# Kernel optimization log

Hardware: AMD Instinct MI355X
Metric: run time of the kernel (lower is better)

## Reference

```python
import jax, jax.numpy as jnp
import numpy as np
from jax.scipy.linalg import expm

NUM_QUBITS = 10
D = 2 ** NUM_QUBITS  # 1024
B, S = 8, 4096


def setup_inputs() -> dict:
    key = jax.random.key(0)
    k_x, k_mr, k_mi = jax.random.split(key, 3)
    inputs = jax.random.normal(k_x, (B, S, D), dtype=jnp.float32)
    M_real = 0.1 * jax.random.normal(k_mr, (D, D), dtype=jnp.float32)
    M_imag = 0.1 * jax.random.normal(k_mi, (D, D), dtype=jnp.float32)
    bias = jnp.zeros((D,), dtype=jnp.float32)
    qubit_gate = jnp.ones((D,), dtype=jnp.float32)
    return {"inputs": inputs, "M_real": M_real, "M_imag": M_imag,
            "bias": bias, "qubit_gate": qubit_gate}


def _l2_normalize(x, axis=-1, eps=1e-12):
    # matches tf.linalg.l2_normalize: x * rsqrt(max(sum(x^2), eps))
    ss = jnp.sum(jnp.square(x), axis=axis, keepdims=True)
    return x * jax.lax.rsqrt(jnp.maximum(ss, eps))


def reference(inputs, M_real, M_imag, bias, qubit_gate):
    norm_inputs = _l2_normalize(inputs, axis=-1)
    A = M_real - M_real.T  # skew-symmetric -> expm(A) is orthogonal
    Bm = M_imag - M_imag.T
    U = expm(A) @ expm(Bm)  # [D, D]
    transformed = jnp.einsum('bsd,de->bse', norm_inputs, U) + bias
    measured = jnp.square(transformed)
    gate_probs = jax.nn.softmax(qubit_gate)  # [D]
    gated_output = measured * gate_probs
    return gated_output, gate_probs
```

## Files before the change

kernel.cpp:

```cpp
#include <hip/hip_runtime.h>


typedef unsigned int u32;
typedef unsigned short u16;
typedef __attribute__((ext_vector_type(8))) short short8;
typedef __attribute__((ext_vector_type(4))) float f32x4;

#define GLOBAL_AS __attribute__((address_space(1)))
#define LDS_AS    __attribute__((address_space(3)))

constexpr int D = 1024;
constexpr float EXPM_SCALE = 1.0f / 4.0f;

__device__ __forceinline__ u16 f2bf(float f) {
  union { float f; u32 u; } v; v.f = f;
  u32 r = (v.u + 0x7FFFu + ((v.u >> 16) & 1u)) >> 16;
  return (u16)r;
}
__device__ __forceinline__ float bf2f(u16 u) {
  union { u32 u; float f; } v; v.u = ((u32)u) << 16;
  return v.f;
}

__device__ __forceinline__ void g2l16(const void* g, void* l) {
  __builtin_amdgcn_global_load_lds((const GLOBAL_AS u32*)g, (LDS_AS u32*)l,
                                   16, 0, 0);
}

#define WAITV(N)                                                   \
  do {                                                             \
    asm volatile("s_waitcnt vmcnt(" #N ")" ::: "memory");          \
    __builtin_amdgcn_sched_barrier(0);                             \
  } while (0)

__device__ void norm_rows8(const float* __restrict__ x, u16* __restrict__ Xn,
                           int r0, int tid, float* sred) {
  float4 v[8];
#pragma unroll
  for (int i = 0; i < 8; ++i)
    v[i] = ((const float4*)(x + (size_t)(r0 + i) * D))[tid];
  float ss[8];
#pragma unroll
  for (int i = 0; i < 8; ++i)
    ss[i] = v[i].x * v[i].x + v[i].y * v[i].y + v[i].z * v[i].z +
            v[i].w * v[i].w;
  for (int o = 32; o; o >>= 1)
#pragma unroll
    for (int i = 0; i < 8; ++i) ss[i] += __shfl_down(ss[i], o);
  const int w = tid >> 6;
  if ((tid & 63) == 0)
#pragma unroll
    for (int i = 0; i < 8; ++i) sred[i * 4 + w] = ss[i];
  __syncthreads();
#pragma unroll
  for (int i = 0; i < 8; ++i) {
    const float tot =
        sred[i * 4 + 0] + sred[i * 4 + 1] + sred[i * 4 + 2] + sred[i * 4 + 3];
    const float inv = rsqrtf(fmaxf(tot, 1e-12f));
    ushort4 o4;
    o4.x = f2bf(v[i].x * inv); o4.y = f2bf(v[i].y * inv);
    o4.z = f2bf(v[i].z * inv); o4.w = f2bf(v[i].w * inv);
    ((ushort4*)(Xn + (size_t)(r0 + i) * D))[tid] = o4;
  }
}

struct SkewParams {
  const float *Mr, *Mi;
  u16 *X0, *X1;
  const float* x;
  u16* Xn;
  int row0;
};
__global__ __launch_bounds__(256) void skew_norm_kernel(SkewParams p) {
  __shared__ __align__(16) float t2[64][67];
  const int bid = blockIdx.x, tid = threadIdx.x;
  if (bid >= 512) {
    norm_rows8(p.x, p.Xn, p.row0 + (bid - 512) * 8, tid, &t2[0][0]);
    return;
  }
  const int z = bid >> 8, t = bid & 255;
  const float* M = z ? p.Mi : p.Mr;
  u16* X = z ? p.X1 : p.X0;
  const int bi = t >> 4, bj = t & 15;
  const int r0 = tid >> 4, c0 = (tid & 15) * 4;
  float4 own[4];
#pragma unroll
  for (int i = 0; i < 4; ++i) {
    const int r = i * 16 + r0;
    own[i] = *(const float4*)(M + (size_t)(bi * 64 + r) * D + bj * 64 + c0);
    const float4 tr =
        *(const float4*)(M + (size_t)(bj * 64 + r) * D + bi * 64 + c0);
    t2[r][c0 + 0] = tr.x; t2[r][c0 + 1] = tr.y;
    t2[r][c0 + 2] = tr.z; t2[r][c0 + 3] = tr.w;
  }
  __syncthreads();
#pragma unroll
  for (int i = 0; i < 4; ++i) {
    const int r = i * 16 + r0;
    const float o[4] = {own[i].x, own[i].y, own[i].z, own[i].w};
    ushort4 hv;
    u16* hp = (u16*)&hv;
#pragma unroll
    for (int j = 0; j < 4; ++j)
      hp[j] = f2bf((o[j] - t2[c0 + j][r]) * EXPM_SCALE);
    *(ushort4*)(X + (size_t)(bi * 64 + r) * D + bj * 64 + c0) = hv;
  }
}

struct CJob {
  const u16 *A, *B;
  const float* C;
  u16 *Dst, *DT;
  float alpha;
};
struct GNParams {
  CJob jobs[2];
  int njobs;
  const float* x;
  u16* Xn;
  int row0;
};
__global__ __launch_bounds__(256) void gemm_norm_kernel(GNParams p) {
  __shared__ __align__(16) u16 ldsA[3][4096];
  __shared__ __align__(16) u16 ldsB[3][4096];
  const int bid = blockIdx.x, tid = threadIdx.x;
  if (bid >= p.njobs) {
    norm_rows8(p.x, p.Xn, p.row0 + (bid - p.njobs) * 8, tid,
               (float*)&ldsA[0][0]);
    return;
  }
  const CJob jb = p.jobs[bid >> 8];
  const int bi = (bid >> 4) & 15, bj = bid & 15;
  const int w = tid >> 6, lane = tid & 63;
  const int wr = w >> 1, wc = w & 1;
  f32x4 acc[2][2];
#pragma unroll
  for (int m = 0; m < 2; ++m)
#pragma unroll
    for (int n = 0; n < 2; ++n) acc[m][n] = f32x4{0.f, 0.f, 0.f, 0.f};
  const int r_l = lane >> 3, c_l = lane & 7;

  auto stage = [&](int buf, int kt) {
    const int k0 = kt * 64;
#pragma unroll
    for (int pp = 0; pp < 2; ++pp) {
      const int row = pp * 32 + w * 8 + r_l;
      const int chunk = c_l ^ (row & 7);
      g2l16(jb.A + (size_t)(bi * 64 + row) * D + k0 + chunk * 8,
            (char*)&ldsA[buf][0] + pp * 4096 + w * 1024);
      g2l16(jb.B + (size_t)(bj * 64 + row) * D + k0 + chunk * 8,
            (char*)&ldsB[buf][0] + pp * 4096 + w * 1024);
    }
  };
  auto compute = [&](int buf) {
#pragma unroll
    for (int h = 0; h < 2; ++h) {
      const int kk = h * 32 + (lane >> 4) * 8;
      short8 a[2], b[2];
#pragma unroll
      for (int m = 0; m < 2; ++m) {
        const int row = wr * 32 + m * 16 + (lane & 15);
        const int off = row * 128 + ((kk * 2) ^ ((row & 7) << 4));
        a[m] = *(const short8*)((const char*)&ldsA[buf][0] + off);
      }
#pragma unroll
      for (int n = 0; n < 2; ++n) {
        const int row = wc * 32 + n * 16 + (lane & 15);
        const int off = row * 128 + ((kk * 2) ^ ((row & 7) << 4));
        b[n] = *(const short8*)((const char*)&ldsB[buf][0] + off);
      }
#pragma unroll
      for (int m = 0; m < 2; ++m)
#pragma unroll
        for (int n = 0; n < 2; ++n)
          acc[m][n] = __builtin_amdgcn_mfma_f32_16x16x32_bf16(
              a[m], b[n], acc[m][n], 0, 0, 0);
    }
  };

  stage(0, 0); stage(1, 1);
  for (int s = 0; s < 14; ++s) {
    WAITV(4);
    __builtin_amdgcn_s_barrier();
    __builtin_amdgcn_sched_barrier(0);
    stage((s + 2) % 3, s + 2);
    compute(s % 3);
  }
  WAITV(4);
  __builtin_amdgcn_s_barrier();
  __builtin_amdgcn_sched_barrier(0);
  compute(14 % 3);
  WAITV(0);
  __builtin_amdgcn_s_barrier();
  __builtin_amdgcn_sched_barrier(0);
  compute(15 % 3);

  const int or0 = bi * 64 + wr * 32, oc0 = bj * 64 + wc * 32;
#pragma unroll
  for (int m = 0; m < 2; ++m)
#pragma unroll
    for (int n = 0; n < 2; ++n) {
      const int row0 = or0 + m * 16 + (lane >> 4) * 4;
      const int col = oc0 + n * 16 + (lane & 15);
      ushort4 dv;
      u16* dp = (u16*)&dv;
#pragma unroll
      for (int r = 0; r < 4; ++r) {
        float v = acc[m][n][r] * jb.alpha;
        if (jb.C) v += jb.C[(size_t)(row0 + r) * D + col];
        dp[r] = f2bf(v);
        jb.Dst[(size_t)(row0 + r) * D + col] = dp[r];
      }
      if (jb.DT)
        *(ushort4*)(jb.DT + (size_t)col * D + row0) = dv;
    }
}

struct X34Params {
  const u16 *X[2], *X2[2];
  u16 *X3[2], *X4[2], *q1t[2];
  float* q0[2];
  const float* qg;
  float* gate_out;
  const float* x;
  u16* Xn;
  int row0;
};
__global__ __launch_bounds__(256) void x34q_norm_kernel(X34Params p) {
  __shared__ __align__(16) u16 ldsA[3][2048];
  __shared__ __align__(16) u16 ldsB1[3][2048];
  __shared__ __align__(16) u16 ldsB2[3][2048];
  const int bid = blockIdx.x, tid = threadIdx.x;
  if (bid > 512) {
    norm_rows8(p.x, p.Xn, p.row0 + (bid - 513) * 8, tid, (float*)&ldsA[0][0]);
    return;
  }
  if (bid == 512) {
    float* red = (float*)&ldsA[0][0];
    const float4 v = ((const float4*)p.qg)[tid];
    float mx = fmaxf(fmaxf(v.x, v.y), fmaxf(v.z, v.w));
    for (int o = 32; o; o >>= 1) mx = fmaxf(mx, __shfl_xor(mx, o));
    if ((tid & 63) == 0) red[tid >> 6] = mx;
    __syncthreads();
    const float M = fmaxf(fmaxf(red[0], red[1]), fmaxf(red[2], red[3]));
    __syncthreads();
    const float e0 = __expf(v.x - M), e1 = __expf(v.y - M),
                e2 = __expf(v.z - M), e3 = __expf(v.w - M);
    float s = e0 + e1 + e2 + e3;
    for (int o = 32; o; o >>= 1) s += __shfl_xor(s, o);
    if ((tid & 63) == 0) red[tid >> 6] = s;
    __syncthreads();
    const float S = red[0] + red[1] + red[2] + red[3];
    const float4 o4 = {e0 / S, e1 / S, e2 / S, e3 / S};
    ((float4*)p.gate_out)[tid] = o4;
    return;
  }
  const int mz = bid >> 8, t = bid & 255;
  const int bi = t >> 4, bj = t & 15;
  const u16* Ag = p.X2[mz];
  const u16* B1g = p.X[mz];
  const u16* B2g = p.X2[mz];
  const int w = tid >> 6, lane = tid & 63;
  const int wr = w >> 1, wc = w & 1;
  f32x4 acc3[2][2], acc4[2][2];
#pragma unroll
  for (int m = 0; m < 2; ++m)
#pragma unroll
    for (int n = 0; n < 2; ++n) {
      acc3[m][n] = f32x4{0.f, 0.f, 0.f, 0.f};
      acc4[m][n] = f32x4{0.f, 0.f, 0.f, 0.f};
    }
  const int srow = tid >> 2, sc = tid & 3;

  auto stage = [&](int buf, int s) {
    const int k0 = s * 32;
    const int csrc = sc ^ (srow & 3);
    g2l16(Ag + (size_t)(bi * 64 + srow) * D + k0 + csrc * 8,
          (char*)&ldsA[buf][0] + tid * 16);
    g2l16(B1g + (size_t)(bj * 64 + srow) * D + k0 + csrc * 8,
          (char*)&ldsB1[buf][0] + tid * 16);
    g2l16(B2g + (size_t)(bj * 64 + srow) * D + k0 + csrc * 8,
          (char*)&ldsB2[buf][0] + tid * 16);
  };
  const int h4 = lane >> 4;
  auto compute = [&](int buf) {
    short8 a[2], b1[2], b2[2];
#pragma unroll
    for (int m = 0; m < 2; ++m) {
      const int row = wr * 32 + m * 16 + (lane & 15);
      const int off = row * 64 + ((h4 ^ (row & 3)) << 4);
      a[m] = *(const short8*)((const char*)&ldsA[buf][0] + off);
    }
#pragma unroll
    for (int n = 0; n < 2; ++n) {
      const int row = wc * 32 + n * 16 + (lane & 15);
      const int off = row * 64 + ((h4 ^ (row & 3)) << 4);
      b1[n] = *(const short8*)((const char*)&ldsB1[buf][0] + off);
      b2[n] = *(const short8*)((const char*)&ldsB2[buf][0] + off);
    }
#pragma unroll
    for (int m = 0; m < 2; ++m)
#pragma unroll
      for (int n = 0; n < 2; ++n) {
        acc3[m][n] = __builtin_amdgcn_mfma_f32_16x16x32_bf16(
            a[m], b1[n], acc3[m][n], 0, 0, 0);
        acc4[m][n] = __builtin_amdgcn_mfma_f32_16x16x32_bf16(
            a[m], b2[n], acc4[m][n], 0, 0, 0);
      }
  };

  stage(0, 0); stage(1, 1);
  for (int s = 0; s < 30; ++s) {
    WAITV(3);
    __builtin_amdgcn_s_barrier();
    __builtin_amdgcn_sched_barrier(0);
    stage((s + 2) % 3, s + 2);
    compute(s % 3);
  }
  WAITV(3);
  __builtin_amdgcn_s_barrier();
  __builtin_amdgcn_sched_barrier(0);
  compute(30 % 3);
  WAITV(0);
  __builtin_amdgcn_s_barrier();
  __builtin_amdgcn_sched_barrier(0);
  compute(31 % 3);

  const int or0 = bi * 64 + wr * 32, oc0 = bj * 64 + wc * 32;
#pragma unroll
  for (int m = 0; m < 2; ++m)
#pragma unroll
    for (int n = 0; n < 2; ++n) {
      const int row0 = or0 + m * 16 + (lane >> 4) * 4;
      const int col = oc0 + n * 16 + (lane & 15);
#pragma unroll
      for (int r = 0; r < 4; ++r) {
        const size_t idx = (size_t)(row0 + r) * D + col;
        const u16 x3v = f2bf(-acc3[m][n][r]);
        const u16 x4v = f2bf(acc4[m][n][r]);
        p.X3[mz][idx] = x3v;
        p.X4[mz][idx] = x4v;
        const float d = (row0 + r == col) ? 1.f : 0.f;
        const float xf = bf2f(p.X[mz][idx]);
        const float x2f = bf2f(p.X2[mz][idx]);
        const float x3f = bf2f(x3v), x4f = bf2f(x4v);
        p.q0[mz][idx] = d + xf + x2f * 0.5f + x3f * (1.f / 6.f);
        p.q1t[mz][idx] =
            f2bf(d * (1.f / 24.f) - xf * (1.f / 120.f) + x2f * (1.f / 720.f) -
                 x3f * (1.f / 5040.f) + x4f * (1.f / 40320.f));
      }
    }
}

__global__ __launch_bounds__(512, 1) void main_gemm_kernel(
    const u16* __restrict__ Xn, const u16* __restrict__ Wm,
    const float* __restrict__ bias, const float* __restrict__ gate,
    float* __restrict__ out) {
  const int tid = threadIdx.x;
  const int wid = tid >> 6, lane = tid & 63;
  const int wr = wid >> 2, wc = wid & 3;
  __shared__ u16 lds[4 * 16384];
  f32x4 acc[8][4];
#pragma unroll
  for (int m = 0; m < 8; ++m)
#pragma unroll
    for (int n = 0; n < 4; ++n) acc[m][n] = f32x4{0.f, 0.f, 0.f, 0.f};

  const int L = blockIdx.x;
  const int bj = (L >> 3) & 3;
  const int bi = (L & 7) + 8 * (L >> 5);
  const int r_ = tid >> 2;
  const int c_ = tid & 3;

  auto stage = [&](int s) {
    char* base = (char*)lds + (s & 3) * 32768;
#pragma unroll
    for (int pp = 0; pp < 2; ++pp) {
      const int row = pp * 128 + r_;
      const int csrc = c_ ^ ((row >> 1) & 3);
      g2l16(Xn + (size_t)(bi * 256 + row) * D + s * 32 + csrc * 8,
            base + pp * 8192 + tid * 16);
      g2l16(Wm + (size_t)(bj * 256 + row) * D + s * 32 + csrc * 8,
            base + 16384 + pp * 8192 + tid * 16);
    }
  };

  const int h = lane >> 4;
  auto compute = [&](int s) {
    const char* base = (const char*)lds + (s & 3) * 32768;
    short8 a[8], b[4];
#pragma unroll
    for (int m = 0; m < 8; ++m) {
      const int row = wr * 128 + m * 16 + (lane & 15);
      const int off = row * 64 + ((h ^ ((row >> 1) & 3)) << 4);
      a[m] = *(const short8*)(base + off);
    }
#pragma unroll
    for (int n = 0; n < 4; ++n) {
      const int row = wc * 64 + n * 16 + (lane & 15);
      const int off = 16384 + row * 64 + ((h ^ ((row >> 1) & 3)) << 4);
      b[n] = *(const short8*)(base + off);
    }
    __builtin_amdgcn_s_setprio(1);
#pragma unroll
    for (int m = 0; m < 8; ++m)
#pragma unroll
      for (int n = 0; n < 4; ++n)
        acc[m][n] = __builtin_amdgcn_mfma_f32_16x16x32_bf16(a[m], b[n],
                                                            acc[m][n], 0, 0, 0);
    __builtin_amdgcn_s_setprio(0);
  };

  stage(0); stage(1); stage(2);
  for (int s = 0; s < 29; ++s) {
    WAITV(8);
    __builtin_amdgcn_s_barrier();
    __builtin_amdgcn_sched_barrier(0);
    stage(s + 3);
    compute(s);
  }
  WAITV(8);
  __builtin_amdgcn_s_barrier();
  __builtin_amdgcn_sched_barrier(0);
  compute(29);
  WAITV(4);
  __builtin_amdgcn_s_barrier();
  __builtin_amdgcn_sched_barrier(0);
  compute(30);
  WAITV(0);
  __builtin_amdgcn_s_barrier();
  __builtin_amdgcn_sched_barrier(0);
  compute(31);

  const int or0 = bi * 256 + wr * 128, oc0 = bj * 256 + wc * 64;
#pragma unroll
  for (int m = 0; m < 8; ++m)
#pragma unroll
    for (int n = 0; n < 4; ++n) {
      const int col = oc0 + n * 16 + (lane & 15);
      const float bc = bias[col], gc = gate[col];
#pragma unroll
      for (int r = 0; r < 4; ++r) {
        const int row = or0 + m * 16 + (lane >> 4) * 4 + r;
        const float t = acc[m][n][r] + bc;
        out[(size_t)row * D + col] = t * t * gc;
      }
    }
}

extern "C" void kernel_launch(void* const* d_in, const int* in_sizes, int n_in,
                              void* d_out, int out_size, void* d_ws,
                              size_t ws_size, hipStream_t stream) {
  (void)in_sizes; (void)n_in; (void)out_size; (void)ws_size;
  const float* inp = (const float*)d_in[0];
  const float* Mr = (const float*)d_in[1];
  const float* Mi = (const float*)d_in[2];
  const float* bias = (const float*)d_in[3];
  const float* qg = (const float*)d_in[4];
  float* out = (float*)d_out;
  float* gate_out = out + (size_t)32768 * 1024;

  char* ws = (char*)d_ws;
  u16* Xn = (u16*)ws;
  auto slot = [&](int m, int s) -> u16* {
    return (u16*)(ws + 67108864 + (size_t)m * 16777216 + (size_t)s * 2097152);
  };
  auto q0p = [&](int m) -> float* {
    return (float*)(ws + 67108864 + (size_t)m * 16777216 + 12582912);
  };
  u16* W = (u16*)(ws + 100663296);

  int row0 = 0;

  {
    SkewParams sp{Mr, Mi, slot(0, 0), slot(1, 0), inp, Xn, row0};
    skew_norm_kernel<<<512 + 585, 256, 0, stream>>>(sp);
    row0 += 4680;
  }
  GNParams gp{};
  gp.x = inp; gp.Xn = Xn;
  for (int m = 0; m < 2; ++m)
    gp.jobs[m] = CJob{slot(m, 0), slot(m, 0), nullptr, slot(m, 1), nullptr,
                      -1.f};
  gp.njobs = 512; gp.row0 = row0;
  gemm_norm_kernel<<<512 + 585, 256, 0, stream>>>(gp);
  row0 += 4680;
  {
    X34Params xp{};
    for (int m = 0; m < 2; ++m) {
      xp.X[m] = slot(m, 0); xp.X2[m] = slot(m, 1);
      xp.X3[m] = slot(m, 2); xp.X4[m] = slot(m, 3);
      xp.q1t[m] = slot(m, 4); xp.q0[m] = q0p(m);
    }
    xp.qg = qg; xp.gate_out = gate_out;
    xp.x = inp; xp.Xn = Xn; xp.row0 = row0;
    x34q_norm_kernel<<<513 + 585, 256, 0, stream>>>(xp);
    row0 += 4680;
  }
  for (int m = 0; m < 2; ++m)
    gp.jobs[m] = CJob{slot(m, 3), slot(m, 4), q0p(m), slot(m, 0), slot(m, 1),
                      1.f};
  gp.njobs = 512; gp.row0 = row0;
  gemm_norm_kernel<<<512 + 585, 256, 0, stream>>>(gp);
  row0 += 4680;
  for (int m = 0; m < 2; ++m)
    gp.jobs[m] = CJob{slot(m, 0), slot(m, 1), nullptr, slot(m, 2), slot(m, 4),
                      1.f};
  gp.row0 = row0;
  gemm_norm_kernel<<<512 + 585, 256, 0, stream>>>(gp);
  row0 += 4680;
  for (int m = 0; m < 2; ++m)
    gp.jobs[m] = CJob{slot(m, 2), slot(m, 4), nullptr, slot(m, 3), slot(m, 5),
                      1.f};
  gp.row0 = row0;
  gemm_norm_kernel<<<512 + 585, 256, 0, stream>>>(gp);
  row0 += 4680;
  gp.jobs[0] = CJob{slot(1, 5), slot(0, 3), nullptr, W, nullptr, 1.f};
  gp.njobs = 256; gp.row0 = row0;
  gemm_norm_kernel<<<256 + 586, 256, 0, stream>>>(gp);

  main_gemm_kernel<<<512, 512, 0, stream>>>(Xn, W, bias, gate_out, out);
}
```

Measured before the change: 204.8 us.

## Load B operand directly from global into registers, shrink LDS pipeline

The W (B) tiles no longer go through LDS. Each wave loads its MFMA B fragments straight from global memory into double-buffered registers. The A tiles keep using LDS with a 3-stage ring instead of 4, which cuts LDS footprint and LDS read traffic. The cost is that B is read from global redundantly by the two wave rows, using uncoalesced 16-byte-per-lane loads, and the waitcnt accounting now mixes register and LDS-directed loads, so latency hiding may be weaker.

```diff
diff --git a/kernel.cpp b/kernel.cpp
--- a/kernel.cpp
+++ b/kernel.cpp
@@ -359,7 +359,7 @@
   const int tid = threadIdx.x;
   const int wid = tid >> 6, lane = tid & 63;
   const int wr = wid >> 2, wc = wid & 3;
-  __shared__ u16 lds[4 * 16384];
+  __shared__ u16 ldsA[3][8192];
   f32x4 acc[8][4];
 #pragma unroll
   for (int m = 0; m < 8; ++m)
@@ -371,36 +371,38 @@
   const int bi = (L & 7) + 8 * (L >> 5);
   const int r_ = tid >> 2;
   const int c_ = tid & 3;
-
-  auto stage = [&](int s) {
-    char* base = (char*)lds + (s & 3) * 32768;
+  const int h = lane >> 4;
+
+  const u16* Bbase[4];
+#pragma unroll
+  for (int n = 0; n < 4; ++n)
+    Bbase[n] = Wm + (size_t)(bj * 256 + wc * 64 + n * 16 + (lane & 15)) * D +
+               h * 8;
+
+  auto stageA = [&](int s) {
+    char* base = (char*)&ldsA[s % 3][0];
 #pragma unroll
     for (int pp = 0; pp < 2; ++pp) {
       const int row = pp * 128 + r_;
       const int csrc = c_ ^ ((row >> 1) & 3);
       g2l16(Xn + (size_t)(bi * 256 + row) * D + s * 32 + csrc * 8,
             base + pp * 8192 + tid * 16);
-      g2l16(Wm + (size_t)(bj * 256 + row) * D + s * 32 + csrc * 8,
-            base + 16384 + pp * 8192 + tid * 16);
-    }
-  };
-
-  const int h = lane >> 4;
-  auto compute = [&](int s) {
-    const char* base = (const char*)lds + (s & 3) * 32768;
-    short8 a[8], b[4];
+    }
+  };
+  auto loadB = [&](int s, short8* breg) {
+#pragma unroll
+    for (int n = 0; n < 4; ++n)
+      breg[n] = *(const short8*)(Bbase[n] + s * 32);
+  };
+  auto compute = [&](int s, const short8* b) {
+    const char* base = (const char*)&ldsA[s % 3][0];
+    short8 a[8];
 #pragma unroll
     for (int m = 0; m < 8; ++m) {
       const int row = wr * 128 + m * 16 + (lane & 15);
       const int off = row * 64 + ((h ^ ((row >> 1) & 3)) << 4);
       a[m] = *(const short8*)(base + off);
     }
-#pragma unroll
-    for (int n = 0; n < 4; ++n) {
-      const int row = wc * 64 + n * 16 + (lane & 15);
-      const int off = 16384 + row * 64 + ((h ^ ((row >> 1) & 3)) << 4);
-      b[n] = *(const short8*)(base + off);
-    }
     __builtin_amdgcn_s_setprio(1);
 #pragma unroll
     for (int m = 0; m < 8; ++m)
@@ -411,26 +413,33 @@
     __builtin_amdgcn_s_setprio(0);
   };
 
-  stage(0); stage(1); stage(2);
-  for (int s = 0; s < 29; ++s) {
-    WAITV(8);
+  short8 bregA[4], bregB[4];
+  loadB(0, bregA);
+  stageA(0);
+  stageA(1);
+  for (int s2 = 0; s2 < 30; s2 += 2) {
+    WAITV(2);
     __builtin_amdgcn_s_barrier();
     __builtin_amdgcn_sched_barrier(0);
-    stage(s + 3);
-    compute(s);
-  }
-  WAITV(8);
+    loadB(s2 + 1, bregB);
+    stageA(s2 + 2);
+    compute(s2, bregA);
+    WAITV(2);
+    __builtin_amdgcn_s_barrier();
+    __builtin_amdgcn_sched_barrier(0);
+    loadB(s2 + 2, bregA);
+    stageA(s2 + 3);
+    compute(s2 + 1, bregB);
+  }
+  WAITV(2);
   __builtin_amdgcn_s_barrier();
   __builtin_amdgcn_sched_barrier(0);
-  compute(29);
-  WAITV(4);
-  __builtin_amdgcn_s_barrier();
-  __builtin_amdgcn_sched_barrier(0);
-  compute(30);
+  loadB(31, bregB);
+  compute(30, bregA);
   WAITV(0);
   __builtin_amdgcn_s_barrier();
   __builtin_amdgcn_sched_barrier(0);
-  compute(31);
+  compute(31, bregB);
 
   const int or0 = bi * 256 + wr * 128, oc0 = bj * 256 + wc * 64;
 #pragma unroll
```

Measured after the change: 239.0 us. 1.17x slower.
